# Kernel optimization log

Hardware: AMD Instinct MI355X
Metric: run time of the kernel (lower is better)

The kernel has to match this reference:

```python
import jax, jax.numpy as jnp
import numpy as np

EPS = 1e-6
NUM_HEADS = 16
ROPE_THETA = 100000.0


def _rope_tables(seq_len, head_dim, theta):
    inv_freq = 1.0 / (theta ** (np.arange(0, head_dim, 2, dtype=np.float32) / head_dim))
    t = np.arange(seq_len, dtype=np.float32)
    freqs = np.outer(t, inv_freq)                      # (S, head_dim//2)
    emb = np.concatenate([freqs, freqs], axis=-1)      # (S, head_dim)
    return jnp.asarray(np.cos(emb))[None], jnp.asarray(np.sin(emb))[None]  # (1,S,D)


def setup_inputs() -> dict:
    key = jax.random.key(0)
    ks = jax.random.split(key, 6)
    B, S, H = 2, 2048, 1024
    head_dim = H // NUM_HEADS
    cos, sin = _rope_tables(S, head_dim, ROPE_THETA)
    scale = 0.02
    return {
        "hidden_states": jax.random.normal(ks[0], (B, S, H), dtype=jnp.float32),
        "cos": cos, "sin": sin,
        "Wq": jax.random.normal(ks[1], (H, H), dtype=jnp.float32) * scale,
        "bq": jnp.zeros((H,), dtype=jnp.float32),
        "Wk": jax.random.normal(ks[2], (H, H), dtype=jnp.float32) * scale,
        "bk": jnp.zeros((H,), dtype=jnp.float32),
        "Wv": jax.random.normal(ks[3], (H, H), dtype=jnp.float32) * scale,
        "bv": jnp.zeros((H,), dtype=jnp.float32),
        "Wo": jax.random.normal(ks[4], (H, H), dtype=jnp.float32) * scale,
        "bo": jnp.zeros((H,), dtype=jnp.float32),
        "rms_weight": jnp.ones((H,), dtype=jnp.float32),
    }


def _rms_norm(x, w):
    var = jnp.mean(x * x, axis=-1, keepdims=True)
    return x * jax.lax.rsqrt(var + EPS) * w


def _rotate_half(x):
    x1, x2 = jnp.split(x, 2, axis=-1)
    return jnp.concatenate([-x2, x1], axis=-1)


def reference(hidden_states, cos, sin, Wq, bq, Wk, bk, Wv, bv, Wo, bo, rms_weight):
    B, S, H = hidden_states.shape
    D = H // NUM_HEADS
    q = hidden_states @ Wq.T + bq
    k = hidden_states @ Wk.T + bk
    v = hidden_states @ Wv.T + bv
    # RMSNorm over full hidden dim BEFORE head split (as in original)
    q = _rms_norm(q, rms_weight)
    k = _rms_norm(k, rms_weight)
    # (B,S,H) -> (B,heads,S,D)
    q = q.reshape(B, S, NUM_HEADS, D).transpose(0, 2, 1, 3)
    k = k.reshape(B, S, NUM_HEADS, D).transpose(0, 2, 1, 3)
    v = v.reshape(B, S, NUM_HEADS, D).transpose(0, 2, 1, 3)
    # RoPE: cos/sin (1,S,D) -> unsqueeze head dim
    c = cos[:, None, :, :]
    s = sin[:, None, :, :]
    q = q * c + _rotate_half(q) * s
    k = k * c + _rotate_half(k) * s
    # attention (faithful: boolean tril mask is ADDED as 0/1, not -inf)
    scale = D ** 0.5
    scores = jnp.einsum("bhqd,bhkd->bhqk", q, k) / scale
    mask = jnp.tril(jnp.ones((S, S), dtype=scores.dtype))  # +1 on causal, +0 elsewhere
    attn = jax.nn.softmax(scores + mask, axis=-1)
    out = jnp.einsum("bhqk,bhkd->bhqd", attn, v)
    out = out.transpose(0, 2, 1, 3).reshape(B, S, H)
    return out @ Wo.T + bo
```

## Files before the change

### kernel.cpp

```cpp
#include <hip/hip_runtime.h>

typedef unsigned short u16;
typedef __attribute__((ext_vector_type(8))) _Float16 half8;
typedef __attribute__((ext_vector_type(2))) __fp16 fp16x2;
typedef __attribute__((ext_vector_type(4))) float f32x4;

#define MFMAH(A,B,C) __builtin_amdgcn_mfma_f32_16x16x32_f16(A,B,C,0,0,0)
#define LOG2E 1.4426950408889634f
#define C1 0.18033688011112042f

__device__ __forceinline__ u16 f2h(float f){
  _Float16 h = (_Float16)f; u16 r; __builtin_memcpy(&r,&h,2); return r;
}
__device__ __forceinline__ float h2f(u16 v){
  _Float16 h; __builtin_memcpy(&h,&v,2); return (float)h;
}
__device__ __forceinline__ unsigned int pack_h2(float a, float b){
  fp16x2 h = __builtin_amdgcn_cvt_pkrtz(a,b);
  unsigned int r; __builtin_memcpy(&r,&h,4); return r;
}

__device__ __forceinline__ void async_ld16(const void* g, void* l) {
  __builtin_amdgcn_global_load_lds(
      (const __attribute__((address_space(1))) unsigned int*)g,
      (__attribute__((address_space(3))) unsigned int*)l, 16, 0, 0);
}

__global__ __launch_bounds__(256) void cast_all(const float* __restrict__ hs,
    const float* __restrict__ wq, const float* __restrict__ wk,
    const float* __restrict__ wv, const float* __restrict__ wo,
    u16* __restrict__ dst)
{
  unsigned int i = blockIdx.x*256 + threadIdx.x;
  size_t el = (size_t)i * 8;
  const float* src; size_t off;
  if (el < 4194304) { src = hs; off = el; }
  else {
    unsigned int r = (unsigned int)((el - 4194304) >> 20);
    src = (r==0)?wq:(r==1)?wk:(r==2)?wv:wo;
    off = (el - 4194304) & 1048575;
  }
  float4 a = *reinterpret_cast<const float4*>(src+off);
  float4 b = *reinterpret_cast<const float4*>(src+off+4);
  uint4 o = {pack_h2(a.x,a.y), pack_h2(a.z,a.w), pack_h2(b.x,b.y), pack_h2(b.z,b.w)};
  *reinterpret_cast<uint4*>(dst + el) = o;
}

__global__ __launch_bounds__(256) void gemm_qk(const u16* __restrict__ A,
                                               const u16* __restrict__ W,
                                               const float* __restrict__ bqp,
                                               const float* __restrict__ bkp,
                                               u16* __restrict__ qout,
                                               u16* __restrict__ kout,
                                               int M, int N, int K)
{
  __shared__ __align__(16) u16 lds_a[128*32];
  __shared__ __align__(16) u16 lds_w[128*32];
  const int t = threadIdx.x;
  const int lane = t & 63, wave = t >> 6;
  const int wm = wave >> 1, wn = wave & 1;
  const int lr = lane & 15, quad = lane >> 4;
  const int n0 = blockIdx.x * 128, m0 = blockIdx.y * 128;
  const int wbase = t & 192;

  const f32x4 fzero = {0.f,0.f,0.f,0.f};
  f32x4 acc[4][4];
  #pragma unroll
  for (int i=0;i<4;++i)
    #pragma unroll
    for (int j=0;j<4;++j) acc[i][j] = fzero;

  for (int k0 = 0; k0 < K; k0 += 32) {
    __syncthreads();
    #pragma unroll
    for (int it=0; it<2; ++it) {
      int idx = it*256 + t;
      int row = idx >> 2, c8 = (idx & 3) * 8;
      int lbase = (it*256 + wbase) * 8;
      async_ld16(&A[(size_t)(m0+row)*K + k0 + c8], &lds_a[lbase]);
      async_ld16(&W[(size_t)(n0+row)*K + k0 + c8], &lds_w[lbase]);
    }
    __syncthreads();
    half8 af[4], bfr[4];
    #pragma unroll
    for (int mt=0; mt<4; ++mt)
      af[mt] = *reinterpret_cast<const half8*>(&lds_a[(wm*64 + mt*16 + lr)*32 + quad*8]);
    #pragma unroll
    for (int nt=0; nt<4; ++nt)
      bfr[nt] = *reinterpret_cast<const half8*>(&lds_w[(wn*64 + nt*16 + lr)*32 + quad*8]);
    #pragma unroll
    for (int mt=0; mt<4; ++mt)
      #pragma unroll
      for (int nt=0; nt<4; ++nt)
        acc[mt][nt] = MFMAH(bfr[nt], af[mt], acc[mt][nt]);
  }

  int which = n0 >> 10;
  const float* bp = which ? bkp : bqp;
  u16* dst = which ? kout : qout;
  #pragma unroll
  for (int nt=0; nt<4; ++nt) {
    int nn = (n0 & 1023) + wn*64 + nt*16 + quad*4;
    float4 bv = *reinterpret_cast<const float4*>(&bp[nn]);
    int hh = nn >> 6, d4 = nn & 63;
    #pragma unroll
    for (int mt=0; mt<4; ++mt) {
      int m = m0 + wm*64 + mt*16 + lr;
      int b = m >> 11, s = m & 2047;
      uint2 o = {pack_h2(acc[mt][nt][0]+bv.x, acc[mt][nt][1]+bv.y),
                 pack_h2(acc[mt][nt][2]+bv.z, acc[mt][nt][3]+bv.w)};
      *reinterpret_cast<uint2*>(&dst[((size_t)(b*16 + hh)*2048 + s)*64 + d4]) = o;
    }
  }
}

__global__ __launch_bounds__(256) void gemm_v(const u16* __restrict__ A,
                                              const u16* __restrict__ W,
                                              const float* __restrict__ bvp,
                                              u16* __restrict__ vout,
                                              int M, int N, int K)
{
  __shared__ __align__(16) u16 lds_a[128*32];
  __shared__ __align__(16) u16 lds_w[128*32];
  const int t = threadIdx.x;
  const int lane = t & 63, wave = t >> 6;
  const int wm = wave >> 1, wn = wave & 1;
  const int lr = lane & 15, quad = lane >> 4;
  const int n0 = blockIdx.x * 128, m0 = blockIdx.y * 128;
  const int wbase = t & 192;

  const f32x4 fzero = {0.f,0.f,0.f,0.f};
  f32x4 acc[4][4];
  #pragma unroll
  for (int i=0;i<4;++i)
    #pragma unroll
    for (int j=0;j<4;++j) acc[i][j] = fzero;

  for (int k0 = 0; k0 < K; k0 += 32) {
    __syncthreads();
    #pragma unroll
    for (int it=0; it<2; ++it) {
      int idx = it*256 + t;
      int row = idx >> 2, c8 = (idx & 3) * 8;
      int lbase = (it*256 + wbase) * 8;
      async_ld16(&A[(size_t)(m0+row)*K + k0 + c8], &lds_a[lbase]);
      async_ld16(&W[(size_t)(n0+row)*K + k0 + c8], &lds_w[lbase]);
    }
    __syncthreads();
    half8 af[4], bfr[4];
    #pragma unroll
    for (int mt=0; mt<4; ++mt)
      af[mt] = *reinterpret_cast<const half8*>(&lds_a[(wm*64 + mt*16 + lr)*32 + quad*8]);
    #pragma unroll
    for (int nt=0; nt<4; ++nt)
      bfr[nt] = *reinterpret_cast<const half8*>(&lds_w[(wn*64 + nt*16 + lr)*32 + quad*8]);
    #pragma unroll
    for (int mt=0; mt<4; ++mt)
      #pragma unroll
      for (int nt=0; nt<4; ++nt)
        acc[mt][nt] = MFMAH(af[mt], bfr[nt], acc[mt][nt]);
  }

  #pragma unroll
  for (int nt=0; nt<4; ++nt) {
    int nn = n0 + wn*64 + nt*16 + lr;
    float bv = bvp[nn];
    int hh = nn >> 6, d = nn & 63;
    #pragma unroll
    for (int mt=0; mt<4; ++mt) {
      int m = m0 + wm*64 + mt*16 + quad*4;
      int b = m >> 11, s = m & 2047;
      uint2 o = {pack_h2(acc[mt][nt][0]+bv, acc[mt][nt][1]+bv),
                 pack_h2(acc[mt][nt][2]+bv, acc[mt][nt][3]+bv)};
      *reinterpret_cast<uint2*>(&vout[((size_t)(b*16 + hh)*64 + d)*2048 + s]) = o;
    }
  }
}

__global__ __launch_bounds__(256) void gemm_o(const u16* __restrict__ A,
                                              const u16* __restrict__ W,
                                              const float* __restrict__ bias,
                                              float* __restrict__ O,
                                              int M, int N, int K)
{
  __shared__ __align__(16) u16 lds_a[128*32];
  __shared__ __align__(16) u16 lds_w[64*32];
  const int t = threadIdx.x;
  const int lane = t & 63, wm = t >> 6;
  const int lr = lane & 15, quad = lane >> 4;
  const int n0 = blockIdx.x * 64, m0 = blockIdx.y * 128;
  const int wbase = t & 192;

  const f32x4 fzero = {0.f,0.f,0.f,0.f};
  f32x4 acc[2][4];
  #pragma unroll
  for (int i=0;i<2;++i)
    #pragma unroll
    for (int j=0;j<4;++j) acc[i][j] = fzero;

  for (int k0 = 0; k0 < K; k0 += 32) {
    __syncthreads();
    #pragma unroll
    for (int it=0; it<2; ++it) {
      int idx = it*256 + t;
      int row = idx >> 2, c8 = (idx & 3) * 8;
      int lbase = (it*256 + wbase) * 8;
      async_ld16(&A[(size_t)(m0+row)*K + k0 + c8], &lds_a[lbase]);
    }
    async_ld16(&W[(size_t)(n0 + (t>>2))*K + k0 + (t&3)*8], &lds_w[wbase*8]);
    __syncthreads();
    half8 af[2], bfr[4];
    #pragma unroll
    for (int mt=0; mt<2; ++mt)
      af[mt] = *reinterpret_cast<const half8*>(&lds_a[(wm*32 + mt*16 + lr)*32 + quad*8]);
    #pragma unroll
    for (int nt=0; nt<4; ++nt)
      bfr[nt] = *reinterpret_cast<const half8*>(&lds_w[(nt*16 + lr)*32 + quad*8]);
    #pragma unroll
    for (int mt=0; mt<2; ++mt)
      #pragma unroll
      for (int nt=0; nt<4; ++nt)
        acc[mt][nt] = MFMAH(bfr[nt], af[mt], acc[mt][nt]);
  }

  #pragma unroll
  for (int nt=0; nt<4; ++nt) {
    int nb = n0 + nt*16 + quad*4;
    float4 bv = *reinterpret_cast<const float4*>(&bias[nb]);
    #pragma unroll
    for (int mt=0; mt<2; ++mt) {
      int m = m0 + wm*32 + mt*16 + lr;
      float4 o = {acc[mt][nt][0]+bv.x, acc[mt][nt][1]+bv.y,
                  acc[mt][nt][2]+bv.z, acc[mt][nt][3]+bv.w};
      *reinterpret_cast<float4*>(&O[(size_t)m * N + nb]) = o;
    }
  }
}

__global__ __launch_bounds__(128) void rmsrope(u16* __restrict__ qb, u16* __restrict__ kb,
                                               const float* __restrict__ cosb,
                                               const float* __restrict__ sinb,
                                               const float* __restrict__ w)
{
  u16* buf = blockIdx.y ? kb : qb;
  const int bs = blockIdx.x;
  const int b = bs >> 11, s = bs & 2047;
  const int t = threadIdx.x;
  const int h = t >> 3, d0 = (t & 7) * 4;
  size_t base = ((size_t)(b*16+h)*2048 + s)*64;

  uint2 u1 = *reinterpret_cast<const uint2*>(&buf[base + d0]);
  uint2 u2 = *reinterpret_cast<const uint2*>(&buf[base + d0 + 32]);
  u16 a1[4], a2[4];
  __builtin_memcpy(a1, &u1, 8); __builtin_memcpy(a2, &u2, 8);
  float x1[4], x2[4];
  float ss = 0.f;
  #pragma unroll
  for (int j=0;j<4;++j){
    x1[j] = h2f(a1[j]); x2[j] = h2f(a2[j]);
    ss += x1[j]*x1[j] + x2[j]*x2[j];
  }
  #pragma unroll
  for (int off=32; off>0; off>>=1) ss += __shfl_xor(ss, off, 64);
  __shared__ float red[2];
  if ((t & 63) == 0) red[t>>6] = ss;
  __syncthreads();
  float tot = red[0] + red[1];
  float r = rsqrtf(tot * (1.0f/1024.0f) + 1e-6f);

  float4 w1 = *reinterpret_cast<const float4*>(&w[h*64+d0]);
  float4 w2 = *reinterpret_cast<const float4*>(&w[h*64+d0+32]);
  float4 c1 = *reinterpret_cast<const float4*>(&cosb[s*64+d0]);
  float4 s1 = *reinterpret_cast<const float4*>(&sinb[s*64+d0]);
  float4 c2 = *reinterpret_cast<const float4*>(&cosb[s*64+d0+32]);
  float4 s2 = *reinterpret_cast<const float4*>(&sinb[s*64+d0+32]);
  float n1[4] = {x1[0]*r*w1.x, x1[1]*r*w1.y, x1[2]*r*w1.z, x1[3]*r*w1.w};
  float n2[4] = {x2[0]*r*w2.x, x2[1]*r*w2.y, x2[2]*r*w2.z, x2[3]*r*w2.w};
  float o1[4] = {n1[0]*c1.x - n2[0]*s1.x, n1[1]*c1.y - n2[1]*s1.y,
                 n1[2]*c1.z - n2[2]*s1.z, n1[3]*c1.w - n2[3]*s1.w};
  float o2[4] = {n2[0]*c2.x + n1[0]*s2.x, n2[1]*c2.y + n1[1]*s2.y,
                 n2[2]*c2.z + n1[2]*s2.z, n2[3]*c2.w + n1[3]*s2.w};
  uint2 v1 = {pack_h2(o1[0],o1[1]), pack_h2(o1[2],o1[3])};
  uint2 v2 = {pack_h2(o2[0],o2[1]), pack_h2(o2[2],o2[3])};
  *reinterpret_cast<uint2*>(&buf[base + d0])      = v1;
  *reinterpret_cast<uint2*>(&buf[base + d0 + 32]) = v2;
}

__global__ __launch_bounds__(512) void attn(const u16* __restrict__ qh,
                                            const u16* __restrict__ kh,
                                            const u16* __restrict__ vt,
                                            u16* __restrict__ ao)
{
  __shared__ __align__(16) u16 kbuf[2][64*72];
  __shared__ __align__(16) u16 vbuf[2][64*72];
  const int t = threadIdx.x;
  const int lane = t & 63, w = t >> 6;
  const int lr = lane & 15, quad = lane >> 4;
  const int bx = blockIdx.x;
  const int qbase = bx * 128;
  const int bh = blockIdx.y;
  const int b = bh >> 4, h = bh & 15;
  const size_t hb = (size_t)bh * 2048 * 64;
  const u16* qp = qh + hb;
  const u16* kp = kh + hb;
  const u16* vtp = vt + hb;

  const int q_abs = qbase + w*16 + lr;
  half8 qf0 = *reinterpret_cast<const half8*>(&qp[(size_t)q_abs*64 + quad*8]);
  half8 qf1 = *reinterpret_cast<const half8*>(&qp[(size_t)q_abs*64 + 32 + quad*8]);

  const int row = t >> 3;
  const int cc = t & 7;
  const int vu = cc >> 2, vq = cc & 3;
  const int k1 = vu*32 + vq*4;
  const int kofs = row*72 + cc*8;
  const u16* kg = kp + (size_t)row*64 + cc*8;
  const u16* vg = vtp + (size_t)row*2048 + k1;

  const f32x4 fzero = {0.f,0.f,0.f,0.f};
  f32x4 oacc[4];
  #pragma unroll
  for (int i=0;i<4;++i) oacc[i] = fzero;
  float lsum = 0.f;
  const int diag = (qbase + w*16) >> 6;

  {
    uint4 kv = *reinterpret_cast<const uint4*>(kg);
    uint2 g1 = *reinterpret_cast<const uint2*>(vg);
    uint2 g2 = *reinterpret_cast<const uint2*>(vg + 16);
    *reinterpret_cast<uint4*>(&kbuf[0][kofs]) = kv;
    uint4 vv = {g1.x, g1.y, g2.x, g2.y};
    *reinterpret_cast<uint4*>(&vbuf[0][kofs]) = vv;
  }

  for (int kt=0; kt<32; ++kt) {
    uint4 kvn; uint2 g1n, g2n;
    if (kt < 31) {
      kvn = *reinterpret_cast<const uint4*>(kg + (size_t)(kt+1)*4096);
      g1n = *reinterpret_cast<const uint2*>(vg + (kt+1)*64);
      g2n = *reinterpret_cast<const uint2*>(vg + (kt+1)*64 + 16);
    }
    __syncthreads();
    const u16* kb = kbuf[kt & 1];
    const u16* vb = vbuf[kt & 1];

    f32x4 zz[4];
    #pragma unroll
    for (int ksub=0; ksub<4; ++ksub) {
      const u16* kr = &kb[(ksub*16+lr)*72 + quad*8];
      half8 a0, a1;
      __builtin_memcpy(&a0, kr, 16);
      __builtin_memcpy(&a1, kr+32, 16);
      f32x4 z = fzero;
      z = MFMAH(a0, qf0, z);
      z = MFMAH(a1, qf1, z);
      zz[ksub] = z;
    }

    unsigned int pk[4][2];
    if (kt != diag) {
      float ml = (kt < diag) ? LOG2E : 0.0f;
      #pragma unroll
      for (int ksub=0; ksub<4; ++ksub) {
        float p0 = __builtin_amdgcn_exp2f(__builtin_fmaf(zz[ksub][0], C1, ml));
        float p1 = __builtin_amdgcn_exp2f(__builtin_fmaf(zz[ksub][1], C1, ml));
        float p2 = __builtin_amdgcn_exp2f(__builtin_fmaf(zz[ksub][2], C1, ml));
        float p3 = __builtin_amdgcn_exp2f(__builtin_fmaf(zz[ksub][3], C1, ml));
        lsum += (p0+p1) + (p2+p3);
        pk[ksub][0] = pack_h2(p0, p1);
        pk[ksub][1] = pack_h2(p2, p3);
      }
    } else {
      #pragma unroll
      for (int ksub=0; ksub<4; ++ksub) {
        int key0 = kt*64 + ksub*16 + quad*4;
        float p[4];
        #pragma unroll
        for (int r=0; r<4; ++r) {
          float ml = (key0 + r <= q_abs) ? LOG2E : 0.0f;
          p[r] = __builtin_amdgcn_exp2f(__builtin_fmaf(zz[ksub][r], C1, ml));
          lsum += p[r];
        }
        pk[ksub][0] = pack_h2(p[0], p[1]);
        pk[ksub][1] = pack_h2(p[2], p[3]);
      }
    }

    #pragma unroll
    for (int u=0; u<2; ++u) {
      uint4 pq = {pk[2*u][0], pk[2*u][1], pk[2*u+1][0], pk[2*u+1][1]};
      half8 pf;
      __builtin_memcpy(&pf, &pq, 16);
      #pragma unroll
      for (int dt=0; dt<4; ++dt) {
        half8 vf;
        __builtin_memcpy(&vf, &vb[(dt*16+lr)*72 + u*32 + quad*8], 16);
        oacc[dt] = MFMAH(vf, pf, oacc[dt]);
      }
    }

    if (kt < 31) {
      *reinterpret_cast<uint4*>(&kbuf[(kt+1)&1][kofs]) = kvn;
      uint4 vv = {g1n.x, g1n.y, g2n.x, g2n.y};
      *reinterpret_cast<uint4*>(&vbuf[(kt+1)&1][kofs]) = vv;
    }
  }

  lsum += __shfl_xor(lsum, 16, 64);
  lsum += __shfl_xor(lsum, 32, 64);
  float inv = 1.0f / lsum;
  size_t rowbase = ((size_t)(b*2048 + q_abs))*1024 + h*64;
  #pragma unroll
  for (int dt=0; dt<4; ++dt) {
    uint2 o = {pack_h2(oacc[dt][0]*inv, oacc[dt][1]*inv),
               pack_h2(oacc[dt][2]*inv, oacc[dt][3]*inv)};
    *reinterpret_cast<uint2*>(&ao[rowbase + dt*16 + quad*4]) = o;
  }
}

extern "C" void kernel_launch(void* const* d_in, const int* in_sizes, int n_in,
                              void* d_out, int out_size, void* d_ws, size_t ws_size,
                              hipStream_t stream)
{
  const float* hs   = (const float*)d_in[0];
  const float* cosb = (const float*)d_in[1];
  const float* sinb = (const float*)d_in[2];
  const float* Wq   = (const float*)d_in[3];
  const float* bq   = (const float*)d_in[4];
  const float* Wk   = (const float*)d_in[5];
  const float* bk   = (const float*)d_in[6];
  const float* Wv   = (const float*)d_in[7];
  const float* bv   = (const float*)d_in[8];
  const float* Wo   = (const float*)d_in[9];
  const float* bo   = (const float*)d_in[10];
  const float* rw   = (const float*)d_in[11];

  const size_t NEL = (size_t)4096 * 1024;
  const size_t WEL = (size_t)1024 * 1024;
  u16* hsb = (u16*)d_ws;
  u16* wqb = hsb + NEL;
  u16* wvb = wqb + 2*WEL;
  u16* wob = wqb + 3*WEL;
  u16* qhb = wob + WEL;
  u16* khb = qhb + NEL;
  u16* vtb = khb + NEL;
  u16* aob = hsb;

  cast_all<<<4096, 256, 0, stream>>>(hs, Wq, Wk, Wv, Wo, hsb);
  gemm_qk<<<dim3(16,32), 256, 0, stream>>>(hsb, wqb, bq, bk, qhb, khb, 4096, 2048, 1024);
  gemm_v<<<dim3(8,32), 256, 0, stream>>>(hsb, wvb, bv, vtb, 4096, 1024, 1024);
  rmsrope<<<dim3(4096,2), 128, 0, stream>>>(qhb, khb, cosb, sinb, rw);
  attn<<<dim3(16,32), 512, 0, stream>>>(qhb, khb, vtb, aob);
  gemm_o<<<dim3(16,32), 256, 0, stream>>>(aob, wob, bo, (float*)d_out, 4096, 1024, 1024);
}
```

Before: 234.5 us.

## Merge QKV GEMMs into one launch and switch attention to 32x32 MFMA tiles

The Q/K and V projection GEMMs become a single kernel with a 24-wide grid that branches on the output column block. The attention kernel moves from 8 waves with 16x16x32 MFMA to 4 waves of 32 query rows each, using 32x32x16 MFMA. Each thread now loads twice as much K/V per tile. This cuts a launch and gives more work per wave with better MFMA efficiency, at the cost of more registers per thread and fewer waves per block to hide latency.

```diff
diff --git a/kernel.cpp b/kernel.cpp
--- a/kernel.cpp
+++ b/kernel.cpp
@@ -4,8 +4,10 @@
 typedef __attribute__((ext_vector_type(8))) _Float16 half8;
 typedef __attribute__((ext_vector_type(2))) __fp16 fp16x2;
 typedef __attribute__((ext_vector_type(4))) float f32x4;
+typedef __attribute__((ext_vector_type(16))) float f32x16;
 
 #define MFMAH(A,B,C) __builtin_amdgcn_mfma_f32_16x16x32_f16(A,B,C,0,0,0)
+#define MFMA32(A,B,C) __builtin_amdgcn_mfma_f32_32x32x16_f16(A,B,C,0,0,0)
 #define LOG2E 1.4426950408889634f
 #define C1 0.18033688011112042f
 
@@ -46,13 +48,15 @@
   *reinterpret_cast<uint4*>(dst + el) = o;
 }
 
-__global__ __launch_bounds__(256) void gemm_qk(const u16* __restrict__ A,
-                                               const u16* __restrict__ W,
-                                               const float* __restrict__ bqp,
-                                               const float* __restrict__ bkp,
-                                               u16* __restrict__ qout,
-                                               u16* __restrict__ kout,
-                                               int M, int N, int K)
+__global__ __launch_bounds__(256) void gemm_qkv(const u16* __restrict__ A,
+                                                const u16* __restrict__ W,
+                                                const float* __restrict__ bqp,
+                                                const float* __restrict__ bkp,
+                                                const float* __restrict__ bvp,
+                                                u16* __restrict__ qout,
+                                                u16* __restrict__ kout,
+                                                u16* __restrict__ vout,
+                                                int M, int K)
 {
   __shared__ __align__(16) u16 lds_a[128*32];
   __shared__ __align__(16) u16 lds_w[128*32];
@@ -62,6 +66,7 @@
   const int lr = lane & 15, quad = lane >> 4;
   const int n0 = blockIdx.x * 128, m0 = blockIdx.y * 128;
   const int wbase = t & 192;
+  const int which = n0 >> 10;
 
   const f32x4 fzero = {0.f,0.f,0.f,0.f};
   f32x4 acc[4][4];
@@ -70,109 +75,85 @@
     #pragma unroll
     for (int j=0;j<4;++j) acc[i][j] = fzero;
 
-  for (int k0 = 0; k0 < K; k0 += 32) {
-    __syncthreads();
-    #pragma unroll
-    for (int it=0; it<2; ++it) {
-      int idx = it*256 + t;
-      int row = idx >> 2, c8 = (idx & 3) * 8;
-      int lbase = (it*256 + wbase) * 8;
-      async_ld16(&A[(size_t)(m0+row)*K + k0 + c8], &lds_a[lbase]);
-      async_ld16(&W[(size_t)(n0+row)*K + k0 + c8], &lds_w[lbase]);
-    }
-    __syncthreads();
-    half8 af[4], bfr[4];
-    #pragma unroll
-    for (int mt=0; mt<4; ++mt)
-      af[mt] = *reinterpret_cast<const half8*>(&lds_a[(wm*64 + mt*16 + lr)*32 + quad*8]);
-    #pragma unroll
-    for (int nt=0; nt<4; ++nt)
-      bfr[nt] = *reinterpret_cast<const half8*>(&lds_w[(wn*64 + nt*16 + lr)*32 + quad*8]);
-    #pragma unroll
-    for (int mt=0; mt<4; ++mt)
+  if (which < 2) {
+    for (int k0 = 0; k0 < K; k0 += 32) {
+      __syncthreads();
+      #pragma unroll
+      for (int it=0; it<2; ++it) {
+        int idx = it*256 + t;
+        int row = idx >> 2, c8 = (idx & 3) * 8;
+        int lbase = (it*256 + wbase) * 8;
+        async_ld16(&A[(size_t)(m0+row)*K + k0 + c8], &lds_a[lbase]);
+        async_ld16(&W[(size_t)(n0+row)*K + k0 + c8], &lds_w[lbase]);
+      }
+      __syncthreads();
+      half8 af[4], bfr[4];
+      #pragma unroll
+      for (int mt=0; mt<4; ++mt)
+        af[mt] = *reinterpret_cast<const half8*>(&lds_a[(wm*64 + mt*16 + lr)*32 + quad*8]);
       #pragma unroll
       for (int nt=0; nt<4; ++nt)
-        acc[mt][nt] = MFMAH(bfr[nt], af[mt], acc[mt][nt]);
-  }
-
-  int which = n0 >> 10;
-  const float* bp = which ? bkp : bqp;
-  u16* dst = which ? kout : qout;
-  #pragma unroll
-  for (int nt=0; nt<4; ++nt) {
-    int nn = (n0 & 1023) + wn*64 + nt*16 + quad*4;
-    float4 bv = *reinterpret_cast<const float4*>(&bp[nn]);
-    int hh = nn >> 6, d4 = nn & 63;
-    #pragma unroll
-    for (int mt=0; mt<4; ++mt) {
-      int m = m0 + wm*64 + mt*16 + lr;
-      int b = m >> 11, s = m & 2047;
-      uint2 o = {pack_h2(acc[mt][nt][0]+bv.x, acc[mt][nt][1]+bv.y),
-                 pack_h2(acc[mt][nt][2]+bv.z, acc[mt][nt][3]+bv.w)};
-      *reinterpret_cast<uint2*>(&dst[((size_t)(b*16 + hh)*2048 + s)*64 + d4]) = o;
-    }
-  }
-}
-
-__global__ __launch_bounds__(256) void gemm_v(const u16* __restrict__ A,
-                                              const u16* __restrict__ W,
-                                              const float* __restrict__ bvp,
-                                              u16* __restrict__ vout,
-                                              int M, int N, int K)
-{
-  __shared__ __align__(16) u16 lds_a[128*32];
-  __shared__ __align__(16) u16 lds_w[128*32];
-  const int t = threadIdx.x;
-  const int lane = t & 63, wave = t >> 6;
-  const int wm = wave >> 1, wn = wave & 1;
-  const int lr = lane & 15, quad = lane >> 4;
-  const int n0 = blockIdx.x * 128, m0 = blockIdx.y * 128;
-  const int wbase = t & 192;
-
-  const f32x4 fzero = {0.f,0.f,0.f,0.f};
-  f32x4 acc[4][4];
-  #pragma unroll
-  for (int i=0;i<4;++i)
-    #pragma unroll
-    for (int j=0;j<4;++j) acc[i][j] = fzero;
-
-  for (int k0 = 0; k0 < K; k0 += 32) {
-    __syncthreads();
-    #pragma unroll
-    for (int it=0; it<2; ++it) {
-      int idx = it*256 + t;
-      int row = idx >> 2, c8 = (idx & 3) * 8;
-      int lbase = (it*256 + wbase) * 8;
-      async_ld16(&A[(size_t)(m0+row)*K + k0 + c8], &lds_a[lbase]);
-      async_ld16(&W[(size_t)(n0+row)*K + k0 + c8], &lds_w[lbase]);
-    }
-    __syncthreads();
-    half8 af[4], bfr[4];
-    #pragma unroll
-    for (int mt=0; mt<4; ++mt)
-      af[mt] = *reinterpret_cast<const half8*>(&lds_a[(wm*64 + mt*16 + lr)*32 + quad*8]);
-    #pragma unroll
-    for (int nt=0; nt<4; ++nt)
-      bfr[nt] = *reinterpret_cast<const half8*>(&lds_w[(wn*64 + nt*16 + lr)*32 + quad*8]);
-    #pragma unroll
-    for (int mt=0; mt<4; ++mt)
+        bfr[nt] = *reinterpret_cast<const half8*>(&lds_w[(wn*64 + nt*16 + lr)*32 + quad*8]);
+      #pragma unroll
+      for (int mt=0; mt<4; ++mt)
+        #pragma unroll
+        for (int nt=0; nt<4; ++nt)
+          acc[mt][nt] = MFMAH(bfr[nt], af[mt], acc[mt][nt]);
+    }
+    const float* bp = which ? bkp : bqp;
+    u16* dst = which ? kout : qout;
+    #pragma unroll
+    for (int nt=0; nt<4; ++nt) {
+      int nn = (n0 & 1023) + wn*64 + nt*16 + quad*4;
+      float4 bv = *reinterpret_cast<const float4*>(&bp[nn]);
+      int hh = nn >> 6, d4 = nn & 63;
+      #pragma unroll
+      for (int mt=0; mt<4; ++mt) {
+        int m = m0 + wm*64 + mt*16 + lr;
+        int b = m >> 11, s = m & 2047;
+        uint2 o = {pack_h2(acc[mt][nt][0]+bv.x, acc[mt][nt][1]+bv.y),
+                   pack_h2(acc[mt][nt][2]+bv.z, acc[mt][nt][3]+bv.w)};
+        *reinterpret_cast<uint2*>(&dst[((size_t)(b*16 + hh)*2048 + s)*64 + d4]) = o;
+      }
+    }
+  } else {
+    for (int k0 = 0; k0 < K; k0 += 32) {
+      __syncthreads();
+      #pragma unroll
+      for (int it=0; it<2; ++it) {
+        int idx = it*256 + t;
+        int row = idx >> 2, c8 = (idx & 3) * 8;
+        int lbase = (it*256 + wbase) * 8;
+        async_ld16(&A[(size_t)(m0+row)*K + k0 + c8], &lds_a[lbase]);
+        async_ld16(&W[(size_t)(n0+row)*K + k0 + c8], &lds_w[lbase]);
+      }
+      __syncthreads();
+      half8 af[4], bfr[4];
+      #pragma unroll
+      for (int mt=0; mt<4; ++mt)
+        af[mt] = *reinterpret_cast<const half8*>(&lds_a[(wm*64 + mt*16 + lr)*32 + quad*8]);
       #pragma unroll
       for (int nt=0; nt<4; ++nt)
-        acc[mt][nt] = MFMAH(af[mt], bfr[nt], acc[mt][nt]);
-  }
-
-  #pragma unroll
-  for (int nt=0; nt<4; ++nt) {
-    int nn = n0 + wn*64 + nt*16 + lr;
-    float bv = bvp[nn];
-    int hh = nn >> 6, d = nn & 63;
-    #pragma unroll
-    for (int mt=0; mt<4; ++mt) {
-      int m = m0 + wm*64 + mt*16 + quad*4;
-      int b = m >> 11, s = m & 2047;
-      uint2 o = {pack_h2(acc[mt][nt][0]+bv, acc[mt][nt][1]+bv),
-                 pack_h2(acc[mt][nt][2]+bv, acc[mt][nt][3]+bv)};
-      *reinterpret_cast<uint2*>(&vout[((size_t)(b*16 + hh)*64 + d)*2048 + s]) = o;
+        bfr[nt] = *reinterpret_cast<const half8*>(&lds_w[(wn*64 + nt*16 + lr)*32 + quad*8]);
+      #pragma unroll
+      for (int mt=0; mt<4; ++mt)
+        #pragma unroll
+        for (int nt=0; nt<4; ++nt)
+          acc[mt][nt] = MFMAH(af[mt], bfr[nt], acc[mt][nt]);
+    }
+    #pragma unroll
+    for (int nt=0; nt<4; ++nt) {
+      int nn = (n0 & 1023) + wn*64 + nt*16 + lr;
+      float bv = bvp[nn];
+      int hh = nn >> 6, d = nn & 63;
+      #pragma unroll
+      for (int mt=0; mt<4; ++mt) {
+        int m = m0 + wm*64 + mt*16 + quad*4;
+        int b = m >> 11, s = m & 2047;
+        uint2 o = {pack_h2(acc[mt][nt][0]+bv, acc[mt][nt][1]+bv),
+                   pack_h2(acc[mt][nt][2]+bv, acc[mt][nt][3]+bv)};
+        *reinterpret_cast<uint2*>(&vout[((size_t)(b*16 + hh)*64 + d)*2048 + s]) = o;
+      }
     }
   }
 }
@@ -286,7 +267,7 @@
   *reinterpret_cast<uint2*>(&buf[base + d0 + 32]) = v2;
 }
 
-__global__ __launch_bounds__(512) void attn(const u16* __restrict__ qh,
+__global__ __launch_bounds__(256) void attn(const u16* __restrict__ qh,
                                             const u16* __restrict__ kh,
                                             const u16* __restrict__ vt,
                                             u16* __restrict__ ao)
@@ -295,9 +276,8 @@
   __shared__ __align__(16) u16 vbuf[2][64*72];
   const int t = threadIdx.x;
   const int lane = t & 63, w = t >> 6;
-  const int lr = lane & 15, quad = lane >> 4;
-  const int bx = blockIdx.x;
-  const int qbase = bx * 128;
+  const int ql = lane & 31, hf = lane >> 5;
+  const int qbase = blockIdx.x * 128;
   const int bh = blockIdx.y;
   const int b = bh >> 4, h = bh & 15;
   const size_t hb = (size_t)bh * 2048 * 64;
@@ -305,117 +285,126 @@
   const u16* kp = kh + hb;
   const u16* vtp = vt + hb;
 
-  const int q_abs = qbase + w*16 + lr;
-  half8 qf0 = *reinterpret_cast<const half8*>(&qp[(size_t)q_abs*64 + quad*8]);
-  half8 qf1 = *reinterpret_cast<const half8*>(&qp[(size_t)q_abs*64 + 32 + quad*8]);
+  const int q_abs = qbase + w*32 + ql;
+  half8 qf[4];
+  #pragma unroll
+  for (int s=0;s<4;++s)
+    qf[s] = *reinterpret_cast<const half8*>(&qp[(size_t)q_abs*64 + s*16 + hf*8]);
 
   const int row = t >> 3;
   const int cc = t & 7;
-  const int vu = cc >> 2, vq = cc & 3;
-  const int k1 = vu*32 + vq*4;
+  const int base2 = 32*(cc>>2) + 16*((cc>>1)&1) + 4*(cc&1);
   const int kofs = row*72 + cc*8;
   const u16* kg = kp + (size_t)row*64 + cc*8;
-  const u16* vg = vtp + (size_t)row*2048 + k1;
-
-  const f32x4 fzero = {0.f,0.f,0.f,0.f};
-  f32x4 oacc[4];
-  #pragma unroll
-  for (int i=0;i<4;++i) oacc[i] = fzero;
+  const u16* vg = vtp + (size_t)row*2048 + base2;
+
+  const f32x16 fz16 = {0.f,0.f,0.f,0.f,0.f,0.f,0.f,0.f,0.f,0.f,0.f,0.f,0.f,0.f,0.f,0.f};
+  f32x16 oacc[2];
+  oacc[0] = fz16; oacc[1] = fz16;
   float lsum = 0.f;
-  const int diag = (qbase + w*16) >> 6;
+  const int diag = (qbase + w*32) >> 6;
 
   {
-    uint4 kv = *reinterpret_cast<const uint4*>(kg);
-    uint2 g1 = *reinterpret_cast<const uint2*>(vg);
-    uint2 g2 = *reinterpret_cast<const uint2*>(vg + 16);
-    *reinterpret_cast<uint4*>(&kbuf[0][kofs]) = kv;
-    uint4 vv = {g1.x, g1.y, g2.x, g2.y};
-    *reinterpret_cast<uint4*>(&vbuf[0][kofs]) = vv;
+    uint4 k0v = *reinterpret_cast<const uint4*>(kg);
+    uint4 k1v = *reinterpret_cast<const uint4*>(kg + 32*64);
+    uint2 a0 = *reinterpret_cast<const uint2*>(vg);
+    uint2 a1 = *reinterpret_cast<const uint2*>(vg + 8);
+    uint2 b0 = *reinterpret_cast<const uint2*>(vg + (size_t)32*2048);
+    uint2 b1 = *reinterpret_cast<const uint2*>(vg + (size_t)32*2048 + 8);
+    *reinterpret_cast<uint4*>(&kbuf[0][kofs])        = k0v;
+    *reinterpret_cast<uint4*>(&kbuf[0][kofs+32*72])  = k1v;
+    uint4 v0 = {a0.x,a0.y,a1.x,a1.y};
+    uint4 v1 = {b0.x,b0.y,b1.x,b1.y};
+    *reinterpret_cast<uint4*>(&vbuf[0][kofs])        = v0;
+    *reinterpret_cast<uint4*>(&vbuf[0][kofs+32*72])  = v1;
   }
 
   for (int kt=0; kt<32; ++kt) {
-    uint4 kvn; uint2 g1n, g2n;
+    uint4 k0n, k1n; uint2 a0n, a1n, b0n, b1n;
     if (kt < 31) {
-      kvn = *reinterpret_cast<const uint4*>(kg + (size_t)(kt+1)*4096);
-      g1n = *reinterpret_cast<const uint2*>(vg + (kt+1)*64);
-      g2n = *reinterpret_cast<const uint2*>(vg + (kt+1)*64 + 16);
+      const u16* kgn = kg + (size_t)(kt+1)*4096;
+      const u16* vgn = vg + (kt+1)*64;
+      k0n = *reinterpret_cast<const uint4*>(kgn);
+      k1n = *reinterpret_cast<const uint4*>(kgn + 32*64);
+      a0n = *reinterpret_cast<const uint2*>(vgn);
+      a1n = *reinterpret_cast<const uint2*>(vgn + 8);
+      b0n = *reinterpret_cast<const uint2*>(vgn + (size_t)32*2048);
+      b1n = *reinterpret_cast<const uint2*>(vgn + (size_t)32*2048 + 8);
     }
     __syncthreads();
     const u16* kb = kbuf[kt & 1];
     const u16* vb = vbuf[kt & 1];
 
-    f32x4 zz[4];
-    #pragma unroll
-    for (int ksub=0; ksub<4; ++ksub) {
-      const u16* kr = &kb[(ksub*16+lr)*72 + quad*8];
-      half8 a0, a1;
-      __builtin_memcpy(&a0, kr, 16);
-      __builtin_memcpy(&a1, kr+32, 16);
-      f32x4 z = fzero;
-      z = MFMAH(a0, qf0, z);
-      z = MFMAH(a1, qf1, z);
-      zz[ksub] = z;
-    }
-
-    unsigned int pk[4][2];
-    if (kt != diag) {
-      float ml = (kt < diag) ? LOG2E : 0.0f;
-      #pragma unroll
-      for (int ksub=0; ksub<4; ++ksub) {
-        float p0 = __builtin_amdgcn_exp2f(__builtin_fmaf(zz[ksub][0], C1, ml));
-        float p1 = __builtin_amdgcn_exp2f(__builtin_fmaf(zz[ksub][1], C1, ml));
-        float p2 = __builtin_amdgcn_exp2f(__builtin_fmaf(zz[ksub][2], C1, ml));
-        float p3 = __builtin_amdgcn_exp2f(__builtin_fmaf(zz[ksub][3], C1, ml));
-        lsum += (p0+p1) + (p2+p3);
-        pk[ksub][0] = pack_h2(p0, p1);
-        pk[ksub][1] = pack_h2(p2, p3);
-      }
-    } else {
-      #pragma unroll
-      for (int ksub=0; ksub<4; ++ksub) {
-        int key0 = kt*64 + ksub*16 + quad*4;
-        float p[4];
+    unsigned int pk[4][4];
+    #pragma unroll
+    for (int kh2=0; kh2<2; ++kh2) {
+      f32x16 z = fz16;
+      #pragma unroll
+      for (int s=0;s<4;++s) {
+        half8 kf;
+        __builtin_memcpy(&kf, &kb[(kh2*32+ql)*72 + s*16 + hf*8], 16);
+        z = MFMA32(kf, qf[s], z);
+      }
+      float p[16];
+      if (kt != diag) {
+        float ml = (kt < diag) ? LOG2E : 0.0f;
         #pragma unroll
-        for (int r=0; r<4; ++r) {
-          float ml = (key0 + r <= q_abs) ? LOG2E : 0.0f;
-          p[r] = __builtin_amdgcn_exp2f(__builtin_fmaf(zz[ksub][r], C1, ml));
+        for (int r=0;r<16;++r) {
+          p[r] = __builtin_amdgcn_exp2f(__builtin_fmaf(z[r], C1, ml));
           lsum += p[r];
         }
-        pk[ksub][0] = pack_h2(p[0], p[1]);
-        pk[ksub][1] = pack_h2(p[2], p[3]);
-      }
-    }
-
-    #pragma unroll
-    for (int u=0; u<2; ++u) {
-      uint4 pq = {pk[2*u][0], pk[2*u][1], pk[2*u+1][0], pk[2*u+1][1]};
-      half8 pf;
-      __builtin_memcpy(&pf, &pq, 16);
-      #pragma unroll
-      for (int dt=0; dt<4; ++dt) {
+      } else {
+        #pragma unroll
+        for (int r=0;r<16;++r) {
+          int key = kt*64 + kh2*32 + (r&3) + 8*(r>>2) + 4*hf;
+          float ml = (key <= q_abs) ? LOG2E : 0.0f;
+          p[r] = __builtin_amdgcn_exp2f(__builtin_fmaf(z[r], C1, ml));
+          lsum += p[r];
+        }
+      }
+      #pragma unroll
+      for (int t2=0;t2<2;++t2)
+        #pragma unroll
+        for (int jj=0;jj<4;++jj)
+          pk[kh2*2+t2][jj] = pack_h2(p[t2*8+jj*2], p[t2*8+jj*2+1]);
+    }
+
+    #pragma unroll
+    for (int st=0;st<4;++st) {
+      uint4 pq = {pk[st][0], pk[st][1], pk[st][2], pk[st][3]};
+      half8 pf; __builtin_memcpy(&pf, &pq, 16);
+      #pragma unroll
+      for (int dh=0; dh<2; ++dh) {
         half8 vf;
-        __builtin_memcpy(&vf, &vb[(dt*16+lr)*72 + u*32 + quad*8], 16);
-        oacc[dt] = MFMAH(vf, pf, oacc[dt]);
+        __builtin_memcpy(&vf, &vb[(dh*32+ql)*72 + st*16 + hf*8], 16);
+        oacc[dh] = MFMA32(vf, pf, oacc[dh]);
       }
     }
 
     if (kt < 31) {
-      *reinterpret_cast<uint4*>(&kbuf[(kt+1)&1][kofs]) = kvn;
-      uint4 vv = {g1n.x, g1n.y, g2n.x, g2n.y};
-      *reinterpret_cast<uint4*>(&vbuf[(kt+1)&1][kofs]) = vv;
-    }
-  }
-
-  lsum += __shfl_xor(lsum, 16, 64);
+      u16* kwn = &kbuf[(kt+1)&1][kofs];
+      u16* vwn = &vbuf[(kt+1)&1][kofs];
+      *reinterpret_cast<uint4*>(kwn)         = k0n;
+      *reinterpret_cast<uint4*>(kwn + 32*72) = k1n;
+      uint4 v0 = {a0n.x,a0n.y,a1n.x,a1n.y};
+      uint4 v1 = {b0n.x,b0n.y,b1n.x,b1n.y};
+      *reinterpret_cast<uint4*>(vwn)         = v0;
+      *reinterpret_cast<uint4*>(vwn + 32*72) = v1;
+    }
+  }
+
   lsum += __shfl_xor(lsum, 32, 64);
   float inv = 1.0f / lsum;
   size_t rowbase = ((size_t)(b*2048 + q_abs))*1024 + h*64;
   #pragma unroll
-  for (int dt=0; dt<4; ++dt) {
-    uint2 o = {pack_h2(oacc[dt][0]*inv, oacc[dt][1]*inv),
-               pack_h2(oacc[dt][2]*inv, oacc[dt][3]*inv)};
-    *reinterpret_cast<uint2*>(&ao[rowbase + dt*16 + quad*4]) = o;
-  }
+  for (int dh=0; dh<2; ++dh)
+    #pragma unroll
+    for (int rq=0; rq<4; ++rq) {
+      int dd = dh*32 + 8*rq + 4*hf;
+      uint2 o = {pack_h2(oacc[dh][rq*4+0]*inv, oacc[dh][rq*4+1]*inv),
+                 pack_h2(oacc[dh][rq*4+2]*inv, oacc[dh][rq*4+3]*inv)};
+      *reinterpret_cast<uint2*>(&ao[rowbase + dd]) = o;
+    }
 }
 
 extern "C" void kernel_launch(void* const* d_in, const int* in_sizes, int n_in,
@@ -439,7 +428,6 @@
   const size_t WEL = (size_t)1024 * 1024;
   u16* hsb = (u16*)d_ws;
   u16* wqb = hsb + NEL;
-  u16* wvb = wqb + 2*WEL;
   u16* wob = wqb + 3*WEL;
   u16* qhb = wob + WEL;
   u16* khb = qhb + NEL;
@@ -447,9 +435,8 @@
   u16* aob = hsb;
 
   cast_all<<<4096, 256, 0, stream>>>(hs, Wq, Wk, Wv, Wo, hsb);
-  gemm_qk<<<dim3(16,32), 256, 0, stream>>>(hsb, wqb, bq, bk, qhb, khb, 4096, 2048, 1024);
-  gemm_v<<<dim3(8,32), 256, 0, stream>>>(hsb, wvb, bv, vtb, 4096, 1024, 1024);
+  gemm_qkv<<<dim3(24,32), 256, 0, stream>>>(hsb, wqb, bq, bk, bv, qhb, khb, vtb, 4096, 1024);
   rmsrope<<<dim3(4096,2), 128, 0, stream>>>(qhb, khb, cosb, sinb, rw);
-  attn<<<dim3(16,32), 512, 0, stream>>>(qhb, khb, vtb, aob);
+  attn<<<dim3(16,32), 256, 0, stream>>>(qhb, khb, vtb, aob);
   gemm_o<<<dim3(16,32), 256, 0, stream>>>(aob, wob, bo, (float*)d_out, 4096, 1024, 1024);
 }
```

Measured after the change: 220.1 us. -6.1%, faster.
